# Performance work log

Measured on AMD Instinct MI355X. Metric: run time of the kernel, lower is better.

Reference implementation:

```python
import jax, jax.numpy as jnp
import numpy as np

CELL = 16          # pixels_per_cell
ORI = 6            # orientations
BIN_W = 180.0 / ORI
EPS = 1e-5         # skimage block-norm eps


def setup_inputs() -> dict:
    key = jax.random.key(0)
    x = jax.random.normal(key, (32, 3, 512, 512), dtype=jnp.float32)
    return {"x": x}


def _hog(x):
    # x: (B, 3, H, W) -> per-image HOG feature vector, matching skimage.feature.hog
    img = jnp.transpose(x, (0, 2, 3, 1))
    gray = 0.299 * img[..., 0] + 0.587 * img[..., 1] + 0.114 * img[..., 2]  # (B,H,W)
    B, H, W = gray.shape

    # skimage central-difference gradients with zeroed borders
    g_row = jnp.zeros_like(gray).at[:, 1:-1, :].set(gray[:, 2:, :] - gray[:, :-2, :])
    g_col = jnp.zeros_like(gray).at[:, :, 1:-1].set(gray[:, :, 2:] - gray[:, :, :-2])

    mag = jnp.hypot(g_row, g_col)
    ori = jnp.degrees(jnp.arctan2(g_row, g_col)) % 180.0
    bins = jnp.clip(jnp.floor(ori / BIN_W).astype(jnp.int32), 0, ORI - 1)

    # hard-assigned orientation histogram per 16x16 cell, averaged over cell pixels
    weighted = jax.nn.one_hot(bins, ORI, dtype=mag.dtype) * mag[..., None]  # (B,H,W,ORI)
    ncr, ncc = H // CELL, W // CELL
    cells = weighted.reshape(B, ncr, CELL, ncc, CELL, ORI).sum(axis=(2, 4)) / (CELL * CELL)

    # 2x2-cell blocks with stride 1 cell: (B, nbr, nbc, 2, 2, ORI)
    blocks = jnp.stack(
        [jnp.stack([cells[:, :-1, :-1], cells[:, :-1, 1:]], axis=3),
         jnp.stack([cells[:, 1:, :-1], cells[:, 1:, 1:]], axis=3)],
        axis=3)

    # L2-Hys normalization
    n1 = jnp.sqrt(jnp.sum(blocks * blocks, axis=(3, 4, 5), keepdims=True) + EPS * EPS)
    nb = jnp.minimum(blocks / n1, 0.2)
    n2 = jnp.sqrt(jnp.sum(nb * nb, axis=(3, 4, 5), keepdims=True) + EPS * EPS)
    nb = nb / n2
    return nb.reshape(B, -1).astype(jnp.float32)


def reference(x):
    return _hog(x)
```

## Files before the change

### kernel.cpp

```cpp
#include <hip/hip_runtime.h>
#include <math.h>

#define BATCH 32
#define HH 512
#define WW 512
#define NC 32
#define NORI 6
#define CH 262144

__device__ __forceinline__ int bin_of(float a) {
    const float deg = __fmul_rn(a, 57.29577951308232f);
    float m = fmodf(deg, 180.0f);
    if (m < 0.0f) m = __fadd_rn(m, 180.0f);
    const int b = (int)floorf(__fdiv_rn(m, 30.0f));
    return min(max(b, 0), NORI - 1);
}
__device__ __forceinline__ float ulp_step(float x, int k) {
    const int i = __float_as_int(x);
    int key = (i >= 0) ? i : -(i & 0x7FFFFFFF);
    key += k;
    const int r = (key >= 0) ? key : (int)(0x80000000u | (unsigned)(-key));
    return __int_as_float(r);
}
__device__ __forceinline__ void deposit(float acc[NORI], int bin, float val) {
#pragma unroll
    for (int o = 0; o < NORI; ++o) acc[o] += (bin == o) ? val : 0.0f;
}
__device__ __forceinline__ float gray_comb(float r, float g, float b) {
    return __fadd_rn(__fadd_rn(__fmul_rn(0.299f, r), __fmul_rn(0.587f, g)),
                     __fmul_rn(0.114f, b));
}
__device__ __forceinline__ float gray_i(const float* __restrict__ img, int off) {
    return gray_comb(img[off], img[off + CH], img[off + 2 * CH]);
}
__device__ __forceinline__ float4 gray4(const float* __restrict__ img, int off) {
    const float4 r = *(const float4*)(img + off);
    const float4 g = *(const float4*)(img + off + CH);
    const float4 b = *(const float4*)(img + off + 2 * CH);
    float4 o;
    o.x = gray_comb(r.x, g.x, b.x);
    o.y = gray_comb(r.y, g.y, b.y);
    o.z = gray_comb(r.z, g.z, b.z);
    o.w = gray_comb(r.w, g.w, b.w);
    return o;
}

__device__ __forceinline__ void hot_pixel(float gy, float gx, int bitk,
                                          float acc[NORI], unsigned& ambmask) {
    const float mag = __fsqrt_rn(__fmaf_rn(gy, gy, __fmul_rn(gx, gx)));
    const bool neg = gy < 0.0f;
    const float cy = fabsf(gy);
    const float cx = neg ? -gx : gx;
    const float pa = __fmul_rn(cy, 0.86602540378443864676f);
    const float pb = __fmul_rn(cx, 0.5f);
    const float pc = __fmul_rn(cy, 0.5f);
    const float pd = __fmul_rn(cx, 0.86602540378443864676f);
    const float t1 = __fsub_rn(pa, pb);
    const float t2 = __fsub_rn(pc, pd);
    const float t3 = -cx;
    const float t4 = -__fadd_rn(pc, pd);
    const float t5 = -__fadd_rn(pa, pb);
    int bin = (t1 >= 0.0f) + (t2 >= 0.0f) + (t3 >= 0.0f) +
              (t4 >= 0.0f) + (t5 >= 0.0f);
    const float s = __fmul_rn(mag, 1e-5f);
    const float mn = fminf(fminf(fminf(fabsf(t1), fabsf(t2)),
                                 fminf(fabsf(t3), fabsf(t4))), fabsf(t5));
    bool amb = (mn < s) || (cx < 0.0f && cy < s);
    if (gy == 0.0f) { bin = 0; amb = false; }
    else if (gx == 0.0f) { bin = 3; amb = false; }
    ambmask |= amb ? (1u << bitk) : 0u;
    deposit(acc, bin, amb ? 0.0f : mag);
}

__global__ __launch_bounds__(256) void hog_cells_kernel(const float* __restrict__ x,
                                                        float* __restrict__ part) {
    const int b = blockIdx.z;
    const int tid = threadIdx.x;
    const int wave = tid >> 6, lane = tid & 63;
    const int by = blockIdx.y;
    const int R0 = by * 16 + wave * 4;
    const int C0 = blockIdx.x * 256;
    const int c0 = C0 + lane * 4;
    const float* img = x + (size_t)b * 3 * HH * WW;

    const bool left_blk = (blockIdx.x == 0);
    const int hc = left_blk ? 256 : 255;
    const bool is_h = (lane == (left_blk ? 63 : 0));

    float4 gm1 = gray4(img, max(R0 - 1, 0) * WW + c0);
    float4 g0  = gray4(img, R0 * WW + c0);
    float hcur = is_h ? gray_i(img, R0 * WW + hc) : 0.0f;

    float acc[NORI] = {0, 0, 0, 0, 0, 0};
    unsigned ambmask = 0;

#pragma unroll
    for (int k = 0; k < 4; ++k) {
        const int r = R0 + k;
        const int rn = min(r + 1, HH - 1);
        const float4 gp1 = gray4(img, rn * WW + c0);
        const float hnext = is_h ? gray_i(img, rn * WW + hc) : 0.0f;

        const bool row_ok = (r >= 1) && (r < HH - 1);
        const float gy0 = row_ok ? __fsub_rn(gp1.x, gm1.x) : 0.0f;
        const float gy1 = row_ok ? __fsub_rn(gp1.y, gm1.y) : 0.0f;
        const float gy2 = row_ok ? __fsub_rn(gp1.z, gm1.z) : 0.0f;
        const float gy3 = row_ok ? __fsub_rn(gp1.w, gm1.w) : 0.0f;

        float left  = __shfl(g0.w, (lane + 63) & 63);
        float right = __shfl(g0.x, (lane + 1) & 63);
        if (is_h) { if (left_blk) right = hcur; else left = hcur; }

        float gx0 = __fsub_rn(g0.y, left);
        const float gx1 = __fsub_rn(g0.z, g0.x);
        const float gx2 = __fsub_rn(g0.w, g0.y);
        float gx3 = __fsub_rn(right, g0.z);
        if (c0 == 0) gx0 = 0.0f;
        if (c0 + 3 == WW - 1) gx3 = 0.0f;

        hot_pixel(gy0, gx0, 4 * k + 0, acc, ambmask);
        hot_pixel(gy1, gx1, 4 * k + 1, acc, ambmask);
        hot_pixel(gy2, gx2, 4 * k + 2, acc, ambmask);
        hot_pixel(gy3, gx3, 4 * k + 3, acc, ambmask);

        gm1 = g0; g0 = gp1; hcur = hnext;
    }

    if (__any(ambmask != 0)) {
        unsigned m = ambmask;
        while (m) {
            const int bit = __builtin_ctz(m);
            m &= m - 1;
            const int r = R0 + (bit >> 2);
            const int c = c0 + (bit & 3);
            const int off = r * WW + c;
            const float gy = __fsub_rn(gray_i(img, off + WW), gray_i(img, off - WW));
            const float gx = __fsub_rn(gray_i(img, off + 1), gray_i(img, off - 1));
            const float mag = __fsqrt_rn(__fmaf_rn(gy, gy, __fmul_rn(gx, gx)));
            const float a = atan2f(gy, gx);
            const int bl = bin_of(ulp_step(a, -2));
            const int bh = bin_of(ulp_step(a, +2));
            if (bl == bh) {
                deposit(acc, bl, mag);
            } else {
                const int b0 = bin_of(a);
                const int bo = (b0 == bl) ? bh : bl;
                deposit(acc, b0, __fmul_rn(mag, 0.65f));
                deposit(acc, bo, __fmul_rn(mag, 0.35f));
            }
        }
    }

#pragma unroll
    for (int o = 0; o < NORI; ++o) {
        float v = acc[o];
        v += __shfl_xor(v, 1);
        v += __shfl_xor(v, 2);
        acc[o] = v;
    }
    if ((lane & 3) == 0) {
        const int cell = lane >> 2;
        const int cc = (C0 >> 4) + cell;
        float* pp = part + ((((size_t)b * NC + by) * NC + cc) * 4 + wave) * NORI;
#pragma unroll
        for (int o = 0; o < NORI; ++o) pp[o] = acc[o];
    }
}

__global__ __launch_bounds__(256) void hog_norm_kernel(const float* __restrict__ part,
                                                       float* __restrict__ out) {
    const int idx = blockIdx.x * 256 + threadIdx.x;
    const int total = BATCH * 31 * 31;
    if (idx >= total) return;
    const int bc = idx % 31;
    const int t = idx / 31;
    const int br = t % 31;
    const int b = t / 31;

    float v[24];
#pragma unroll
    for (int i = 0; i < 2; ++i)
#pragma unroll
        for (int j = 0; j < 2; ++j) {
            const float* pp = part + ((((size_t)b * NC + (br + i)) * NC + (bc + j)) * 4) * NORI;
            float s[NORI];
#pragma unroll
            for (int o = 0; o < NORI; ++o)
                s[o] = ((pp[o] + pp[6 + o]) + pp[12 + o]) + pp[18 + o];
#pragma unroll
            for (int o = 0; o < NORI; ++o)
                v[(i * 2 + j) * NORI + o] = s[o] * (1.0f / 256.0f);
        }

    float ss = 0.0f;
#pragma unroll
    for (int k = 0; k < 24; ++k) ss = __fadd_rn(ss, __fmul_rn(v[k], v[k]));
    const float n1 = __fsqrt_rn(__fadd_rn(ss, 1e-10f));
    float ss2 = 0.0f;
#pragma unroll
    for (int k = 0; k < 24; ++k) {
        v[k] = fminf(__fdiv_rn(v[k], n1), 0.2f);
        ss2 = __fadd_rn(ss2, __fmul_rn(v[k], v[k]));
    }
    const float n2 = __fsqrt_rn(__fadd_rn(ss2, 1e-10f));
    float* op = out + (size_t)idx * 24;
#pragma unroll
    for (int k = 0; k < 24; ++k) op[k] = __fdiv_rn(v[k], n2);
}

extern "C" void kernel_launch(void* const* d_in, const int* in_sizes, int n_in,
                              void* d_out, int out_size, void* d_ws, size_t ws_size,
                              hipStream_t stream) {
    const float* x = (const float*)d_in[0];
    float* out = (float*)d_out;
    float* part = (float*)d_ws;

    dim3 g1(2, NC, BATCH), b1(256);
    hog_cells_kernel<<<g1, b1, 0, stream>>>(x, part);

    const int total = BATCH * 31 * 31;
    hog_norm_kernel<<<(total + 255) / 256, 256, 0, stream>>>(part, out);
}
```

Before: 154.1 us.

## Make cells kernel persistent with register double-buffered tile prefetch

The cells kernel becomes a fixed 512-block grid in which each block handles four tiles in turn. Before computing the current tile, it issues the raw RGB loads for the next tile into a second register buffer, so global load latency overlaps with compute. Each wave loads all six input rows at once instead of streaming them row by row. This greatly raises register pressure (two 6-row RGB buffers per thread), which can cut occupancy or cause spills, and the smaller grid leaves less latency hiding to the hardware scheduler.

```diff
diff --git a/kernel.cpp b/kernel.cpp
--- a/kernel.cpp
+++ b/kernel.cpp
@@ -7,6 +7,7 @@
 #define NC 32
 #define NORI 6
 #define CH 262144
+#define NBLK 512
 
 __device__ __forceinline__ int bin_of(float a) {
     const float deg = __fmul_rn(a, 57.29577951308232f);
@@ -32,17 +33,6 @@
 }
 __device__ __forceinline__ float gray_i(const float* __restrict__ img, int off) {
     return gray_comb(img[off], img[off + CH], img[off + 2 * CH]);
-}
-__device__ __forceinline__ float4 gray4(const float* __restrict__ img, int off) {
-    const float4 r = *(const float4*)(img + off);
-    const float4 g = *(const float4*)(img + off + CH);
-    const float4 b = *(const float4*)(img + off + 2 * CH);
-    float4 o;
-    o.x = gray_comb(r.x, g.x, b.x);
-    o.y = gray_comb(r.y, g.y, b.y);
-    o.z = gray_comb(r.z, g.z, b.z);
-    o.w = gray_comb(r.w, g.w, b.w);
-    return o;
 }
 
 __device__ __forceinline__ void hot_pixel(float gy, float gx, int bitk,
@@ -72,98 +62,133 @@
     deposit(acc, bin, amb ? 0.0f : mag);
 }
 
+struct TileRegs {
+    float4 cr[6], cg[6], cb[6];
+    float hr[6], hg[6], hb[6];
+};
+
+__device__ __forceinline__ void load_tile(const float* __restrict__ x,
+                                          int b, int by, int wave,
+                                          int c0, int hc, bool is_h,
+                                          TileRegs& T) {
+    const float* img = x + (size_t)b * 3 * CH;
+    const int R0 = by * 16 + wave * 4;
+#pragma unroll
+    for (int i = 0; i < 6; ++i) {
+        const int roff = min(max(R0 - 1 + i, 0), HH - 1) * WW;
+        T.cr[i] = *(const float4*)(img + roff + c0);
+        T.cg[i] = *(const float4*)(img + roff + c0 + CH);
+        T.cb[i] = *(const float4*)(img + roff + c0 + 2 * CH);
+        T.hr[i] = is_h ? img[roff + hc] : 0.0f;
+        T.hg[i] = is_h ? img[roff + hc + CH] : 0.0f;
+        T.hb[i] = is_h ? img[roff + hc + 2 * CH] : 0.0f;
+    }
+}
+
 __global__ __launch_bounds__(256) void hog_cells_kernel(const float* __restrict__ x,
                                                         float* __restrict__ part) {
-    const int b = blockIdx.z;
     const int tid = threadIdx.x;
     const int wave = tid >> 6, lane = tid & 63;
-    const int by = blockIdx.y;
-    const int R0 = by * 16 + wave * 4;
-    const int C0 = blockIdx.x * 256;
-    const int c0 = C0 + lane * 4;
-    const float* img = x + (size_t)b * 3 * HH * WW;
-
-    const bool left_blk = (blockIdx.x == 0);
+    const int t0 = blockIdx.x;
+    const int bx = t0 & 1;
+    const bool left_blk = (bx == 0);
     const int hc = left_blk ? 256 : 255;
     const bool is_h = (lane == (left_blk ? 63 : 0));
-
-    float4 gm1 = gray4(img, max(R0 - 1, 0) * WW + c0);
-    float4 g0  = gray4(img, R0 * WW + c0);
-    float hcur = is_h ? gray_i(img, R0 * WW + hc) : 0.0f;
-
-    float acc[NORI] = {0, 0, 0, 0, 0, 0};
-    unsigned ambmask = 0;
-
-#pragma unroll
-    for (int k = 0; k < 4; ++k) {
-        const int r = R0 + k;
-        const int rn = min(r + 1, HH - 1);
-        const float4 gp1 = gray4(img, rn * WW + c0);
-        const float hnext = is_h ? gray_i(img, rn * WW + hc) : 0.0f;
-
-        const bool row_ok = (r >= 1) && (r < HH - 1);
-        const float gy0 = row_ok ? __fsub_rn(gp1.x, gm1.x) : 0.0f;
-        const float gy1 = row_ok ? __fsub_rn(gp1.y, gm1.y) : 0.0f;
-        const float gy2 = row_ok ? __fsub_rn(gp1.z, gm1.z) : 0.0f;
-        const float gy3 = row_ok ? __fsub_rn(gp1.w, gm1.w) : 0.0f;
-
-        float left  = __shfl(g0.w, (lane + 63) & 63);
-        float right = __shfl(g0.x, (lane + 1) & 63);
-        if (is_h) { if (left_blk) right = hcur; else left = hcur; }
-
-        float gx0 = __fsub_rn(g0.y, left);
-        const float gx1 = __fsub_rn(g0.z, g0.x);
-        const float gx2 = __fsub_rn(g0.w, g0.y);
-        float gx3 = __fsub_rn(right, g0.z);
-        if (c0 == 0) gx0 = 0.0f;
-        if (c0 + 3 == WW - 1) gx3 = 0.0f;
-
-        hot_pixel(gy0, gx0, 4 * k + 0, acc, ambmask);
-        hot_pixel(gy1, gx1, 4 * k + 1, acc, ambmask);
-        hot_pixel(gy2, gx2, 4 * k + 2, acc, ambmask);
-        hot_pixel(gy3, gx3, 4 * k + 3, acc, ambmask);
-
-        gm1 = g0; g0 = gp1; hcur = hnext;
-    }
-
-    if (__any(ambmask != 0)) {
-        unsigned m = ambmask;
-        while (m) {
-            const int bit = __builtin_ctz(m);
-            m &= m - 1;
-            const int r = R0 + (bit >> 2);
-            const int c = c0 + (bit & 3);
-            const int off = r * WW + c;
-            const float gy = __fsub_rn(gray_i(img, off + WW), gray_i(img, off - WW));
-            const float gx = __fsub_rn(gray_i(img, off + 1), gray_i(img, off - 1));
-            const float mag = __fsqrt_rn(__fmaf_rn(gy, gy, __fmul_rn(gx, gx)));
-            const float a = atan2f(gy, gx);
-            const int bl = bin_of(ulp_step(a, -2));
-            const int bh = bin_of(ulp_step(a, +2));
-            if (bl == bh) {
-                deposit(acc, bl, mag);
-            } else {
-                const int b0 = bin_of(a);
-                const int bo = (b0 == bl) ? bh : bl;
-                deposit(acc, b0, __fmul_rn(mag, 0.65f));
-                deposit(acc, bo, __fmul_rn(mag, 0.35f));
+    const int c0 = bx * 256 + lane * 4;
+
+    TileRegs A, B;
+    int t = t0;
+    int b = t >> 6, by = (t >> 1) & 31;
+    load_tile(x, b, by, wave, c0, hc, is_h, A);
+
+#pragma unroll
+    for (int i = 0; i < 4; ++i) {
+        float4 g[6];
+        float hgray[6];
+#pragma unroll
+        for (int j = 0; j < 6; ++j) {
+            g[j].x = gray_comb(A.cr[j].x, A.cg[j].x, A.cb[j].x);
+            g[j].y = gray_comb(A.cr[j].y, A.cg[j].y, A.cb[j].y);
+            g[j].z = gray_comb(A.cr[j].z, A.cg[j].z, A.cb[j].z);
+            g[j].w = gray_comb(A.cr[j].w, A.cg[j].w, A.cb[j].w);
+            hgray[j] = gray_comb(A.hr[j], A.hg[j], A.hb[j]);
+        }
+
+        const int tn = t + NBLK;
+        const int bn = tn >> 6, byn = (tn >> 1) & 31;
+        if (i < 3) load_tile(x, bn, byn, wave, c0, hc, is_h, B);
+
+        const int R0 = by * 16 + wave * 4;
+        const float* img = x + (size_t)b * 3 * CH;
+        float acc[NORI] = {0, 0, 0, 0, 0, 0};
+        unsigned ambmask = 0;
+#pragma unroll
+        for (int k = 0; k < 4; ++k) {
+            const int r = R0 + k;
+            const bool row_ok = (r >= 1) && (r < HH - 1);
+            const float4 gt = g[k], gc = g[k + 1], gb = g[k + 2];
+            const float gy0 = row_ok ? __fsub_rn(gb.x, gt.x) : 0.0f;
+            const float gy1 = row_ok ? __fsub_rn(gb.y, gt.y) : 0.0f;
+            const float gy2 = row_ok ? __fsub_rn(gb.z, gt.z) : 0.0f;
+            const float gy3 = row_ok ? __fsub_rn(gb.w, gt.w) : 0.0f;
+
+            float left  = __shfl(gc.w, (lane + 63) & 63);
+            float right = __shfl(gc.x, (lane + 1) & 63);
+            if (is_h) { if (left_blk) right = hgray[k + 1]; else left = hgray[k + 1]; }
+
+            float gx0 = __fsub_rn(gc.y, left);
+            const float gx1 = __fsub_rn(gc.z, gc.x);
+            const float gx2 = __fsub_rn(gc.w, gc.y);
+            float gx3 = __fsub_rn(right, gc.z);
+            if (c0 == 0) gx0 = 0.0f;
+            if (c0 + 3 == WW - 1) gx3 = 0.0f;
+
+            hot_pixel(gy0, gx0, 4 * k + 0, acc, ambmask);
+            hot_pixel(gy1, gx1, 4 * k + 1, acc, ambmask);
+            hot_pixel(gy2, gx2, 4 * k + 2, acc, ambmask);
+            hot_pixel(gy3, gx3, 4 * k + 3, acc, ambmask);
+        }
+
+        if (__any(ambmask != 0)) {
+            unsigned m = ambmask;
+            while (m) {
+                const int bit = __builtin_ctz(m);
+                m &= m - 1;
+                const int r = R0 + (bit >> 2);
+                const int c = c0 + (bit & 3);
+                const int off = r * WW + c;
+                const float gy = __fsub_rn(gray_i(img, off + WW), gray_i(img, off - WW));
+                const float gx = __fsub_rn(gray_i(img, off + 1), gray_i(img, off - 1));
+                const float mag = __fsqrt_rn(__fmaf_rn(gy, gy, __fmul_rn(gx, gx)));
+                const float a = atan2f(gy, gx);
+                const int bl = bin_of(ulp_step(a, -2));
+                const int bh = bin_of(ulp_step(a, +2));
+                if (bl == bh) {
+                    deposit(acc, bl, mag);
+                } else {
+                    const int b0 = bin_of(a);
+                    const int bo = (b0 == bl) ? bh : bl;
+                    deposit(acc, b0, __fmul_rn(mag, 0.65f));
+                    deposit(acc, bo, __fmul_rn(mag, 0.35f));
+                }
             }
         }
-    }
-
-#pragma unroll
-    for (int o = 0; o < NORI; ++o) {
-        float v = acc[o];
-        v += __shfl_xor(v, 1);
-        v += __shfl_xor(v, 2);
-        acc[o] = v;
-    }
-    if ((lane & 3) == 0) {
-        const int cell = lane >> 2;
-        const int cc = (C0 >> 4) + cell;
-        float* pp = part + ((((size_t)b * NC + by) * NC + cc) * 4 + wave) * NORI;
-#pragma unroll
-        for (int o = 0; o < NORI; ++o) pp[o] = acc[o];
+
+#pragma unroll
+        for (int o = 0; o < NORI; ++o) {
+            float v = acc[o];
+            v += __shfl_xor(v, 1);
+            v += __shfl_xor(v, 2);
+            acc[o] = v;
+        }
+        if ((lane & 3) == 0) {
+            const int cc = bx * 16 + (lane >> 2);
+            float* pp = part + ((((size_t)b * NC + by) * NC + cc) * 4 + wave) * NORI;
+#pragma unroll
+            for (int o = 0; o < NORI; ++o) pp[o] = acc[o];
+        }
+
+        if (i < 3) { A = B; t = tn; b = bn; by = byn; }
     }
 }
 
@@ -215,8 +240,7 @@
     float* out = (float*)d_out;
     float* part = (float*)d_ws;
 
-    dim3 g1(2, NC, BATCH), b1(256);
-    hog_cells_kernel<<<g1, b1, 0, stream>>>(x, part);
+    hog_cells_kernel<<<NBLK, 256, 0, stream>>>(x, part);
 
     const int total = BATCH * 31 * 31;
     hog_norm_kernel<<<(total + 255) / 256, 256, 0, stream>>>(part, out);
```

After: 167.3 us. 1.09x slower.
